# Kernel tuning notes

Measured on AMD Instinct MI355X. Metric: run time of the kernel, lower is better.

The kernel has to match this reference:

```python
import jax, jax.numpy as jnp
import numpy as np

D = 1024
EPS = 1e-5


def layer_norm(x, w, b):
    mu = jnp.mean(x, axis=-1, keepdims=True)
    var = jnp.var(x, axis=-1, keepdims=True)
    return (x - mu) * jax.lax.rsqrt(var + EPS) * w + b


def setup_inputs() -> dict:
    key = jax.random.key(0)
    ks = jax.random.split(key, 8)
    B, S = 8, 2048
    s_attn = 1.0 / np.sqrt(D)
    s_fc = 1.0 / np.sqrt(D)
    s_proj = 1.0 / np.sqrt(4 * D)
    return {
        "x": jax.random.normal(ks[0], (B, S, D), dtype=jnp.float32),
        "ln1_w": jnp.ones((D,), jnp.float32),
        "ln1_b": jnp.zeros((D,), jnp.float32),
        "W_attn": jax.random.uniform(ks[1], (D, 3 * D), jnp.float32, -s_attn, s_attn),
        "b_attn": jax.random.uniform(ks[2], (3 * D,), jnp.float32, -s_attn, s_attn),
        "ln2_w": jnp.ones((D,), jnp.float32),
        "ln2_b": jnp.zeros((D,), jnp.float32),
        "W_fc": jax.random.uniform(ks[3], (D, 4 * D), jnp.float32, -s_fc, s_fc),
        "b_fc": jax.random.uniform(ks[4], (4 * D,), jnp.float32, -s_fc, s_fc),
        "W_proj": jax.random.uniform(ks[5], (4 * D, D), jnp.float32, -s_proj, s_proj),
        "b_proj": jax.random.uniform(ks[6], (D,), jnp.float32, -s_proj, s_proj),
    }


def reference(x, ln1_w, ln1_b, W_attn, b_attn, ln2_w, ln2_b, W_fc, b_fc, W_proj, b_proj):
    # Attention sub-block (single-head, hand-rolled)
    h = layer_norm(x, ln1_w, ln1_b)                       # [B,S,D]
    qkv = h @ W_attn + b_attn                              # [B,S,3D]
    q, k, v = jnp.split(qkv, 3, axis=2)
    scores = jnp.einsum('bsd,btd->bst', q, k) / jnp.sqrt(jnp.float32(D))
    attn = jax.nn.softmax(scores, axis=-1)                 # [B,S,S]
    x = x + jnp.einsum('bst,btd->bsd', attn, v)            # residual
    # MLP sub-block (no residual in original)
    h = layer_norm(x, ln2_w, ln2_b)
    h = jax.nn.gelu(h @ W_fc + b_fc, approximate=False)    # torch GELU default = erf
    return h @ W_proj + b_proj
```

## Files before the change

kernel.cpp:

```cpp
#include <hip/hip_runtime.h>
#include <hip/hip_bf16.h>
#include <math.h>

#define D_MODEL 1024
#define SEQ 2048
#define BATCH 8

typedef unsigned short u16;
typedef __attribute__((ext_vector_type(8))) short bf16x8;
typedef __attribute__((ext_vector_type(4))) float f32x4;

__device__ inline u16 f2bf(float f) {
  __hip_bfloat16 h = __float2bfloat16(f);
  return __builtin_bit_cast(u16, h);
}
__device__ inline float bf2f(u16 u) {
  return __builtin_bit_cast(float, (unsigned)u << 16);
}

__device__ __forceinline__ void async_cp16(const u16* g, u16* l) {
  __builtin_amdgcn_global_load_lds(
      (const __attribute__((address_space(1))) void*)g,
      (__attribute__((address_space(3))) void*)l, 16, 0, 0);
}

__global__ __launch_bounds__(256) void ln_kernel(
    const float* __restrict__ x, const float* __restrict__ w,
    const float* __restrict__ b, u16* __restrict__ out) {
  int row = blockIdx.x;
  int t = threadIdx.x;
  const float4* xr = (const float4*)(x + (size_t)row * D_MODEL);
  float4 v = xr[t];
  float s = v.x + v.y + v.z + v.w;
  float s2 = v.x * v.x + v.y * v.y + v.z * v.z + v.w * v.w;
  for (int o = 32; o > 0; o >>= 1) {
    s += __shfl_down(s, o);
    s2 += __shfl_down(s2, o);
  }
  __shared__ float red[10];
  int wave = t >> 6, lane = t & 63;
  if (lane == 0) { red[wave] = s; red[4 + wave] = s2; }
  __syncthreads();
  if (t == 0) {
    float S = red[0] + red[1] + red[2] + red[3];
    float S2 = red[4] + red[5] + red[6] + red[7];
    float mu = S * (1.f / D_MODEL);
    float var = S2 * (1.f / D_MODEL) - mu * mu;
    red[8] = mu;
    red[9] = rsqrtf(var + 1e-5f);
  }
  __syncthreads();
  float mu = red[8], rstd = red[9];
  float4 w4 = ((const float4*)w)[t];
  float4 b4 = ((const float4*)b)[t];
  ushort4 o4;
  o4.x = f2bf((v.x - mu) * rstd * w4.x + b4.x);
  o4.y = f2bf((v.y - mu) * rstd * w4.y + b4.y);
  o4.z = f2bf((v.z - mu) * rstd * w4.z + b4.z);
  o4.w = f2bf((v.w - mu) * rstd * w4.w + b4.w);
  ((ushort4*)(out + (size_t)row * D_MODEL))[t] = o4;
}

__global__ __launch_bounds__(256) void softmax_bf16_kernel(u16* __restrict__ p) {
  int row = blockIdx.x;
  int t = threadIdx.x;
  int4 q = ((const int4*)(p + (size_t)row * SEQ))[t];
  u16 us[8];
  __builtin_memcpy(us, &q, 16);
  float vals[8];
  for (int i = 0; i < 8; i++) vals[i] = bf2f(us[i]);
  float m = vals[0];
  for (int i = 1; i < 8; i++) m = fmaxf(m, vals[i]);
  for (int o = 32; o > 0; o >>= 1) m = fmaxf(m, __shfl_down(m, o));
  __shared__ float red[6];
  int wave = t >> 6, lane = t & 63;
  if (lane == 0) red[wave] = m;
  __syncthreads();
  if (t == 0) red[4] = fmaxf(fmaxf(red[0], red[1]), fmaxf(red[2], red[3]));
  __syncthreads();
  m = red[4];
  float s = 0.f;
  for (int i = 0; i < 8; i++) { vals[i] = __expf(vals[i] - m); s += vals[i]; }
  for (int o = 32; o > 0; o >>= 1) s += __shfl_down(s, o);
  if (lane == 0) red[wave] = s;
  __syncthreads();
  if (t == 0) red[5] = red[0] + red[1] + red[2] + red[3];
  __syncthreads();
  float inv = 1.f / red[5];
  union { u16 us[8]; int4 v4; } pk;
  for (int i = 0; i < 8; i++) pk.us[i] = f2bf(vals[i] * inv);
  ((int4*)(p + (size_t)row * SEQ))[t] = pk.v4;
}

__global__ __launch_bounds__(256) void wconv_t(
    const float* __restrict__ W, u16* __restrict__ Wt, int K, int N) {
  int k0 = blockIdx.x * 64, n0 = blockIdx.y * 64;
  __shared__ u16 tile[64][65];
  int t = threadIdx.x;
  for (int p = 0; p < 16; p++) {
    int idx = p * 256 + t;
    int r = idx >> 6, c = idx & 63;
    tile[r][c] = f2bf(W[(size_t)(k0 + r) * N + n0 + c]);
  }
  __syncthreads();
  for (int p = 0; p < 16; p++) {
    int idx = p * 256 + t;
    int r = idx >> 6, c = idx & 63;
    Wt[(size_t)(n0 + r) * K + k0 + c] = tile[c][r];
  }
}

enum { EPI_QKV = 0, EPI_SCALE_BF16 = 1, EPI_RESID_F32 = 2,
       EPI_GELU_BF16 = 3, EPI_BIAS_F32 = 4 };

template <int EPI>
__global__ __launch_bounds__(256, 4) void gemm_bt(
    const u16* __restrict__ A, const u16* __restrict__ Bt,
    void* __restrict__ Cv, const float* __restrict__ bias,
    const float* __restrict__ resid, u16* __restrict__ vTp,
    int M, int N, int K, int lda, int ldb, int ldc, float scale,
    long long saB, long long sbB, long long scB, long long srB) {
  __shared__ __align__(16) u16 lA[128 * 64];
  __shared__ __align__(16) u16 lB[128 * 64];
  int t = threadIdx.x;
  int zb = blockIdx.z;
  A += (size_t)zb * saB;
  Bt += (size_t)zb * sbB;

  int gx = gridDim.x;
  int flat = blockIdx.x + gx * blockIdx.y;
  int rem = flat % (4 * gx);
  int m0 = ((flat / (4 * gx)) * 4 + (rem & 3)) * 128;
  int n0 = (rem >> 2) * 128;

  int wv = t >> 6, lane = t & 63;

  int srow = t >> 3;
  int scg = (t & 7) ^ ((t >> 3) & 7);
  int scol = scg << 3;
  const u16* gA = A + (size_t)(m0 + srow) * lda + scol;
  const u16* gB = Bt + (size_t)(n0 + srow) * ldb + scol;
  u16* lAd = lA + t * 8;
  u16* lBd = lB + t * 8;

  int wm = (wv >> 1) * 64, wn = (wv & 1) * 64;
  int lr = lane & 15, lq = lane >> 4;
  int keyr = lr & 7;
  f32x4 acc[4][4] = {};

  for (int k0 = 0; k0 < K; k0 += 64) {
    #pragma unroll
    for (int r = 0; r < 4; r++) {
      async_cp16(gA + (size_t)(r * 32) * lda, lAd + r * 2048);
      async_cp16(gB + (size_t)(r * 32) * ldb, lBd + r * 2048);
    }
    gA += 64; gB += 64;
    __syncthreads();
    #pragma unroll
    for (int ks = 0; ks < 2; ks++) {
      bf16x8 af[4], bfr[4];
      #pragma unroll
      for (int i = 0; i < 4; i++)
        af[i] = *(const bf16x8*)(lA + (wm + i * 16 + lr) * 64 +
                                 (((lq + 4 * ks) ^ keyr) << 3));
      #pragma unroll
      for (int j = 0; j < 4; j++)
        bfr[j] = *(const bf16x8*)(lB + (wn + j * 16 + lr) * 64 +
                                  (((lq + 4 * ks) ^ keyr) << 3));
      #pragma unroll
      for (int i = 0; i < 4; i++)
        #pragma unroll
        for (int j = 0; j < 4; j++)
          acc[i][j] = __builtin_amdgcn_mfma_f32_16x16x32_bf16(
              af[i], bfr[j], acc[i][j], 0, 0, 0);
    }
    __syncthreads();
  }

  float* Cf = (float*)Cv + (size_t)zb * scB;
  u16* Ch = (u16*)Cv + (size_t)zb * scB;
  const float* rz = resid + (size_t)zb * srB;

  if constexpr (EPI == EPI_QKV) {
    if (n0 >= 2048) {
      for (int i = 0; i < 4; i++) {
        int row0 = m0 + wm + i * 16 + lq * 4;
        int batch = row0 >> 11, s0 = row0 & 2047;
        for (int j = 0; j < 4; j++) {
          int d = n0 - 2048 + wn + j * 16 + lr;
          float bcol = bias[n0 + wn + j * 16 + lr];
          ushort4 o4;
          o4.x = f2bf(acc[i][j][0] + bcol);
          o4.y = f2bf(acc[i][j][1] + bcol);
          o4.z = f2bf(acc[i][j][2] + bcol);
          o4.w = f2bf(acc[i][j][3] + bcol);
          *(ushort4*)(vTp + (((size_t)batch * 1024 + d) << 11) + s0) = o4;
        }
      }
      return;
    }
  }

  for (int i = 0; i < 4; i++) {
    for (int j = 0; j < 4; j++) {
      int col = n0 + wn + j * 16 + lr;
      float bcol = (EPI == EPI_QKV || EPI == EPI_GELU_BF16 ||
                    EPI == EPI_BIAS_F32) ? bias[col] : 0.f;
      for (int r = 0; r < 4; r++) {
        int row = m0 + wm + i * 16 + lq * 4 + r;
        float v = acc[i][j][r];
        size_t off = (size_t)row * ldc + col;
        if constexpr (EPI == EPI_QKV) {
          Ch[off] = f2bf(v + bcol);
        } else if constexpr (EPI == EPI_SCALE_BF16) {
          Ch[off] = f2bf(v * scale);
        } else if constexpr (EPI == EPI_RESID_F32) {
          Cf[off] = v + rz[off];
        } else if constexpr (EPI == EPI_GELU_BF16) {
          float xx = v + bcol;
          float u = xx * (0.7978845608f + 0.0356774081f * xx * xx);
          float e = __expf(2.f * u);
          float th = 1.f - 2.f * __builtin_amdgcn_rcpf(e + 1.f);
          Ch[off] = f2bf(0.5f * xx * (1.f + th));
        } else {
          Cf[off] = v + bcol;
        }
      }
    }
  }
}

extern "C" void kernel_launch(void* const* d_in, const int* in_sizes, int n_in,
                              void* d_out, int out_size, void* d_ws, size_t ws_size,
                              hipStream_t stream) {
  const float* x      = (const float*)d_in[0];
  const float* ln1_w  = (const float*)d_in[1];
  const float* ln1_b  = (const float*)d_in[2];
  const float* W_attn = (const float*)d_in[3];
  const float* b_attn = (const float*)d_in[4];
  const float* ln2_w  = (const float*)d_in[5];
  const float* ln2_b  = (const float*)d_in[6];
  const float* W_fc   = (const float*)d_in[7];
  const float* b_fc   = (const float*)d_in[8];
  const float* W_proj = (const float*)d_in[9];
  const float* b_proj = (const float*)d_in[10];
  float* out = (float*)d_out;

  if (ws_size < 190840832ull) return;
  char* ws = (char*)d_ws;
  u16* hb   = (u16*)(ws + 0);
  u16* qk   = (u16*)(ws + 33554432ull);
  u16* vT   = (u16*)(ws + 100663296ull);
  u16* sc   = (u16*)(ws + 134217728ull);
  u16* fc   = (u16*)(ws + 33554432ull);
  u16* WaT  = (u16*)(ws + 167772160ull);
  u16* WfT  = (u16*)(ws + 174063616ull);
  u16* WpT  = (u16*)(ws + 182452224ull);

  wconv_t<<<dim3(1024 / 64, 3072 / 64), 256, 0, stream>>>(W_attn, WaT, 1024, 3072);
  wconv_t<<<dim3(1024 / 64, 4096 / 64), 256, 0, stream>>>(W_fc, WfT, 1024, 4096);
  wconv_t<<<dim3(4096 / 64, 1024 / 64), 256, 0, stream>>>(W_proj, WpT, 4096, 1024);

  ln_kernel<<<BATCH * SEQ, 256, 0, stream>>>(x, ln1_w, ln1_b, hb);

  gemm_bt<EPI_QKV><<<dim3(24, 128, 1), 256, 0, stream>>>(
      hb, WaT, qk, b_attn, x, vT, BATCH * SEQ, 3072, 1024, 1024, 1024, 2048, 1.f,
      0, 0, 0, 0);

  const float iss = 0.03125f;
  for (int c = 0; c < 2; c++) {
    const u16* qb = qk + (size_t)c * 4 * SEQ * 2048;
    gemm_bt<EPI_SCALE_BF16><<<dim3(16, 16, 4), 256, 0, stream>>>(
        qb, qb + 1024, sc, nullptr, x, nullptr, SEQ, SEQ, 1024, 2048, 2048, SEQ,
        iss, (long long)SEQ * 2048, (long long)SEQ * 2048, (long long)SEQ * SEQ, 0);
    softmax_bf16_kernel<<<4 * SEQ, 256, 0, stream>>>(sc);
    gemm_bt<EPI_RESID_F32><<<dim3(8, 16, 4), 256, 0, stream>>>(
        sc, vT + (size_t)c * 4 * D_MODEL * SEQ,
        out + (size_t)c * 4 * SEQ * D_MODEL, nullptr,
        x + (size_t)c * 4 * SEQ * D_MODEL, nullptr, SEQ, D_MODEL, SEQ,
        SEQ, SEQ, D_MODEL, 1.f,
        (long long)SEQ * SEQ, (long long)D_MODEL * SEQ,
        (long long)SEQ * D_MODEL, (long long)SEQ * D_MODEL);
  }

  ln_kernel<<<BATCH * SEQ, 256, 0, stream>>>(out, ln2_w, ln2_b, hb);

  gemm_bt<EPI_GELU_BF16><<<dim3(32, 128, 1), 256, 0, stream>>>(
      hb, WfT, fc, b_fc, x, nullptr, BATCH * SEQ, 4096, 1024, 1024, 1024, 4096,
      1.f, 0, 0, 0, 0);

  gemm_bt<EPI_BIAS_F32><<<dim3(8, 128, 1), 256, 0, stream>>>(
      fc, WpT, out, b_proj, x, nullptr, BATCH * SEQ, 1024, 4096, 4096, 4096,
      1024, 1.f, 0, 0, 0, 0);
}
```

Baseline: 776.0 us.

## Add 256x256-tile 8-wave pipelined bf16 GEMM and use it for four matmuls

Adds a new GEMM kernel with 256x256 output tiles, 512 threads, and a double-buffered LDS pipeline. Asynchronous global-to-LDS copies are interleaved with MFMA quarters under explicit barriers and priority hints, and a XOR-swizzled LDS layout plus an 8-way workgroup swizzle are used for cache locality. It replaces the older GEMM for the QKV, QK^T, FC and projection matmuls, aiming for more data reuse per tile and better overlap of loads with compute. The large tiles use 128 KB of LDS and many accumulator registers per thread, and launch far fewer workgroups, which risks poor occupancy and tail effects on the smaller batched score GEMM. The hand-tuned waitcnt counts assume a fixed K multiple of 128.

```diff
diff --git a/kernel.cpp b/kernel.cpp
--- a/kernel.cpp
+++ b/kernel.cpp
@@ -230,6 +230,210 @@
   }
 }
 
+#define PHB() do { asm volatile("" ::: "memory");      \
+    __builtin_amdgcn_sched_barrier(0);                 \
+    __builtin_amdgcn_s_barrier();                      \
+    __builtin_amdgcn_sched_barrier(0);                 \
+    asm volatile("" ::: "memory"); } while (0)
+
+#define LDA_(t_, ks_, fi_) \
+  (*(const bf16x8*)(lds + (((t_) & 1) * 4 + (ks_)) * 8192 + aoff + (fi_) * 512))
+#define LDB_(t_, ks_, fj_) \
+  (*(const bf16x8*)(lds + (((t_) & 1) * 4 + 2 + (ks_)) * 8192 + boff + (fj_) * 512))
+
+#define MMQ(base_) do {                                               \
+    __builtin_amdgcn_s_setprio(1);                                    \
+    _Pragma("unroll")                                                 \
+    for (int ii = 0; ii < 4; ii++)                                    \
+      _Pragma("unroll")                                               \
+      for (int jj = 0; jj < 4; jj++)                                  \
+        acc[(base_) + ii][jj] = __builtin_amdgcn_mfma_f32_16x16x32_bf16( \
+            a_[ii], b_[jj], acc[(base_) + ii][jj], 0, 0, 0);          \
+    __builtin_amdgcn_s_setprio(0); } while (0)
+
+template <int EPI>
+__global__ __launch_bounds__(512, 2) void gemm256(
+    const u16* __restrict__ A, const u16* __restrict__ Bt,
+    void* __restrict__ Cv, const float* __restrict__ bias,
+    const float* __restrict__ resid, u16* __restrict__ vTp,
+    int M, int N, int K, int lda, int ldb, int ldc, float scale,
+    long long saB, long long sbB, long long scB, long long srB) {
+  __shared__ __align__(16) u16 lds[65536];
+  int t = threadIdx.x;
+  int zb = blockIdx.z;
+  A += (size_t)zb * saB;
+  Bt += (size_t)zb * sbB;
+
+  int gx = gridDim.x;
+  int nwg = gx * gridDim.y;
+  int flat = blockIdx.x + gx * blockIdx.y;
+  int swz = flat;
+  if (!(nwg & 7)) { int cpx = nwg >> 3; swz = (flat & 7) * cpx + (flat >> 3); }
+  int mt = swz / gx, nt = swz % gx;
+  int m0 = mt * 256, n0 = nt * 256;
+
+  int wv = t >> 6, lane = t & 63, lr = lane & 15, lq = lane >> 4;
+  int wm = (wv >> 2) * 128, wn = (wv & 3) * 64;
+  int pg8 = (lq ^ ((lr >> 1) & 3)) << 3;
+  int aoff = (wm + lr) * 32 + pg8;
+  int boff = (wn + lr) * 32 + pg8;
+
+  int r0 = t >> 2, r1 = r0 + 128;
+  int c0 = ((t & 3) ^ ((r0 >> 1) & 3)) << 3;
+  const u16* gA0 = A + (size_t)(m0 + r0) * lda + c0;
+  const u16* gA1 = A + (size_t)(m0 + r1) * lda + c0;
+  const u16* gB0 = Bt + (size_t)(n0 + r0) * ldb + c0;
+  const u16* gB1 = Bt + (size_t)(n0 + r1) * ldb + c0;
+
+  f32x4 acc[8][4] = {};
+  int NT = K >> 6, NI = NT >> 1;
+
+  auto stage = [&](int tile, int ab, int ks) {
+    int ko = tile * 64 + ks * 32;
+    u16* d = lds + ((tile & 1) * 4 + ab * 2 + ks) * 8192 + t * 8;
+    if (ab) {
+      async_cp16(gB0 + ko, d);
+      async_cp16(gB1 + ko, d + 4096);
+    } else {
+      async_cp16(gA0 + ko, d);
+      async_cp16(gA1 + ko, d + 4096);
+    }
+  };
+
+  stage(0, 0, 0); stage(0, 1, 0); stage(0, 0, 1); stage(0, 1, 1);
+  stage(1, 0, 0); stage(1, 1, 0);
+  asm volatile("s_waitcnt vmcnt(4)" ::: "memory");
+  PHB();
+
+  bf16x8 a_[4], b_[4];
+  for (int it = 0; it < NI; it++) {
+    int ta = 2 * it, tb = ta + 1, tc = ta + 2, td = ta + 3;
+    bool ck = tc < NT, dk = td < NT;
+    bool last = (it == NI - 1);
+
+    #pragma unroll
+    for (int f = 0; f < 4; f++) a_[f] = LDA_(ta, 0, f);
+    #pragma unroll
+    for (int f = 0; f < 4; f++) b_[f] = LDB_(ta, 0, f);
+    stage(tb, 0, 1);
+    PHB();
+    MMQ(0);
+    PHB();
+
+    #pragma unroll
+    for (int f = 0; f < 4; f++) a_[f] = LDA_(ta, 0, 4 + f);
+    stage(tb, 1, 1);
+    PHB();
+    MMQ(4);
+    PHB();
+
+    #pragma unroll
+    for (int f = 0; f < 4; f++) a_[f] = LDA_(ta, 1, f);
+    #pragma unroll
+    for (int f = 0; f < 4; f++) b_[f] = LDB_(ta, 1, f);
+    if (ck) stage(tc, 0, 0);
+    PHB();
+    MMQ(0);
+    PHB();
+
+    #pragma unroll
+    for (int f = 0; f < 4; f++) a_[f] = LDA_(ta, 1, 4 + f);
+    if (ck) stage(tc, 1, 0);
+    PHB();
+    MMQ(4);
+    if (last) { asm volatile("s_waitcnt vmcnt(0)" ::: "memory"); }
+    else      { asm volatile("s_waitcnt vmcnt(4)" ::: "memory"); }
+    PHB();
+
+    #pragma unroll
+    for (int f = 0; f < 4; f++) a_[f] = LDA_(tb, 0, f);
+    #pragma unroll
+    for (int f = 0; f < 4; f++) b_[f] = LDB_(tb, 0, f);
+    if (ck) stage(tc, 0, 1);
+    PHB();
+    MMQ(0);
+    PHB();
+
+    #pragma unroll
+    for (int f = 0; f < 4; f++) a_[f] = LDA_(tb, 0, 4 + f);
+    if (ck) stage(tc, 1, 1);
+    PHB();
+    MMQ(4);
+    PHB();
+
+    #pragma unroll
+    for (int f = 0; f < 4; f++) a_[f] = LDA_(tb, 1, f);
+    #pragma unroll
+    for (int f = 0; f < 4; f++) b_[f] = LDB_(tb, 1, f);
+    if (dk) stage(td, 0, 0);
+    PHB();
+    MMQ(0);
+    PHB();
+
+    #pragma unroll
+    for (int f = 0; f < 4; f++) a_[f] = LDA_(tb, 1, 4 + f);
+    if (dk) stage(td, 1, 0);
+    PHB();
+    MMQ(4);
+    asm volatile("s_waitcnt vmcnt(4)" ::: "memory");
+    PHB();
+  }
+
+  float* Cf = (float*)Cv + (size_t)zb * scB;
+  u16* Ch = (u16*)Cv + (size_t)zb * scB;
+  const float* rz = resid + (size_t)zb * srB;
+
+  if constexpr (EPI == EPI_QKV) {
+    if (n0 >= 2048) {
+      #pragma unroll
+      for (int i = 0; i < 8; i++) {
+        int row0 = m0 + wm + i * 16 + lq * 4;
+        int batch = row0 >> 11, s0 = row0 & 2047;
+        #pragma unroll
+        for (int j = 0; j < 4; j++) {
+          int d = n0 - 2048 + wn + j * 16 + lr;
+          float bcol = bias[n0 + wn + j * 16 + lr];
+          ushort4 o4;
+          o4.x = f2bf(acc[i][j][0] + bcol);
+          o4.y = f2bf(acc[i][j][1] + bcol);
+          o4.z = f2bf(acc[i][j][2] + bcol);
+          o4.w = f2bf(acc[i][j][3] + bcol);
+          *(ushort4*)(vTp + (((size_t)batch * 1024 + d) << 11) + s0) = o4;
+        }
+      }
+      return;
+    }
+  }
+
+  for (int i = 0; i < 8; i++) {
+    for (int j = 0; j < 4; j++) {
+      int col = n0 + wn + j * 16 + lr;
+      float bcol = (EPI == EPI_QKV || EPI == EPI_GELU_BF16 ||
+                    EPI == EPI_BIAS_F32) ? bias[col] : 0.f;
+      for (int r = 0; r < 4; r++) {
+        int row = m0 + wm + i * 16 + lq * 4 + r;
+        float v = acc[i][j][r];
+        size_t off = (size_t)row * ldc + col;
+        if constexpr (EPI == EPI_QKV) {
+          Ch[off] = f2bf(v + bcol);
+        } else if constexpr (EPI == EPI_SCALE_BF16) {
+          Ch[off] = f2bf(v * scale);
+        } else if constexpr (EPI == EPI_RESID_F32) {
+          Cf[off] = v + rz[off];
+        } else if constexpr (EPI == EPI_GELU_BF16) {
+          float xx = v + bcol;
+          float u = xx * (0.7978845608f + 0.0356774081f * xx * xx);
+          float e = __expf(2.f * u);
+          float th = 1.f - 2.f * __builtin_amdgcn_rcpf(e + 1.f);
+          Ch[off] = f2bf(0.5f * xx * (1.f + th));
+        } else {
+          Cf[off] = v + bcol;
+        }
+      }
+    }
+  }
+}
+
 extern "C" void kernel_launch(void* const* d_in, const int* in_sizes, int n_in,
                               void* d_out, int out_size, void* d_ws, size_t ws_size,
                               hipStream_t stream) {
@@ -263,14 +467,14 @@
 
   ln_kernel<<<BATCH * SEQ, 256, 0, stream>>>(x, ln1_w, ln1_b, hb);
 
-  gemm_bt<EPI_QKV><<<dim3(24, 128, 1), 256, 0, stream>>>(
+  gemm256<EPI_QKV><<<dim3(12, 64, 1), 512, 0, stream>>>(
       hb, WaT, qk, b_attn, x, vT, BATCH * SEQ, 3072, 1024, 1024, 1024, 2048, 1.f,
       0, 0, 0, 0);
 
   const float iss = 0.03125f;
   for (int c = 0; c < 2; c++) {
     const u16* qb = qk + (size_t)c * 4 * SEQ * 2048;
-    gemm_bt<EPI_SCALE_BF16><<<dim3(16, 16, 4), 256, 0, stream>>>(
+    gemm256<EPI_SCALE_BF16><<<dim3(8, 8, 4), 512, 0, stream>>>(
         qb, qb + 1024, sc, nullptr, x, nullptr, SEQ, SEQ, 1024, 2048, 2048, SEQ,
         iss, (long long)SEQ * 2048, (long long)SEQ * 2048, (long long)SEQ * SEQ, 0);
     softmax_bf16_kernel<<<4 * SEQ, 256, 0, stream>>>(sc);
@@ -285,11 +489,11 @@
 
   ln_kernel<<<BATCH * SEQ, 256, 0, stream>>>(out, ln2_w, ln2_b, hb);
 
-  gemm_bt<EPI_GELU_BF16><<<dim3(32, 128, 1), 256, 0, stream>>>(
+  gemm256<EPI_GELU_BF16><<<dim3(16, 64, 1), 512, 0, stream>>>(
       hb, WfT, fc, b_fc, x, nullptr, BATCH * SEQ, 4096, 1024, 1024, 1024, 4096,
       1.f, 0, 0, 0, 0);
 
-  gemm_bt<EPI_BIAS_F32><<<dim3(8, 128, 1), 256, 0, stream>>>(
+  gemm256<EPI_BIAS_F32><<<dim3(4, 64, 1), 512, 0, stream>>>(
       fc, WpT, out, b_proj, x, nullptr, BATCH * SEQ, 1024, 4096, 4096, 4096,
       1024, 1.f, 0, 0, 0, 0);
 }
```

After: 756.4 us. -2.5%, faster.
